# Performance work log

Measured on AMD Instinct MI355X. Metric: run time of the kernel, lower is better.

Reference implementation:

```python
import jax, jax.numpy as jnp
import numpy as np

B, IMG, P, D, NH, HS, L, V, TB, MLP, A = 32, 224, 16, 768, 12, 64, 12, 128, 32, 3072, 7
NPATCH = (IMG // P) ** 2          # 196 patches per image
SEQ = 1 + NPATCH + 1 + NPATCH + TB  # 426 = cls + obs + goal_tok + goal + lang


def _ln(x, g, b):
    m = x.mean(-1, keepdims=True)
    v = x.var(-1, keepdims=True)
    return (x - m) / jnp.sqrt(v + 1e-5) * g + b


def _patches(img):
    # einops 'b (h p1) (w p2) c -> b (h w) (p1 p2 c)'
    b = img.shape[0]
    h = IMG // P
    x = img.reshape(b, h, P, h, P, 3).transpose(0, 1, 3, 2, 4, 5)
    return x.reshape(b, h * h, P * P * 3)


def _forward(images, goal_imgs, goals_txt, patch_W, patch_b, tok_emb, pos_emb,
             cls_tok, goal_tok, Wq, Wk, Wv, Wo, bo, ln1_g, ln1_b, ln2_g, ln2_b,
             W1, b1, W2, b2, lnf_g, lnf_b, ah_W1, ah_b1, ah_W2, ah_b2):
    tok_obs = _patches(images) @ patch_W + patch_b        # [B, 196, D]
    tok_goal = _patches(goal_imgs) @ patch_W + patch_b    # [B, 196, D]
    tok_lang = tok_emb[goals_txt]                         # [B, 32, D]
    b = images.shape[0]
    x = jnp.concatenate([
        jnp.broadcast_to(cls_tok, (b, 1, D)),
        tok_obs,
        jnp.broadcast_to(goal_tok, (b, 1, D)),
        tok_goal,
        tok_lang,
    ], axis=1)                                            # [B, SEQ, D]
    x = x + pos_emb[None]
    scale = D ** -0.5  # NOTE: original Head scales by full n_embd, not head_size

    def block(x, p):
        wq, wk, wv, wo, bo_, l1g, l1b, l2g, l2b, w1, b1_, w2, b2_ = p
        xn = _ln(x, l1g, l1b)
        q = jnp.einsum('btd,hde->bhte', xn, wq)
        k = jnp.einsum('btd,hde->bhte', xn, wk)
        v = jnp.einsum('btd,hde->bhte', xn, wv)
        wei = jax.nn.softmax(jnp.einsum('bhte,bhse->bhts', q, k) * scale, axis=-1)
        att = jnp.einsum('bhts,bhse->bhte', wei, v)
        att = att.transpose(0, 2, 1, 3).reshape(x.shape[0], -1, D)  # concat heads
        x = x + att @ wo + bo_
        h = jax.nn.relu(_ln(x, l2g, l2b) @ w1 + b1_)
        x = x + h @ w2 + b2_
        return x, None

    x, _ = jax.lax.scan(block, x, (Wq, Wk, Wv, Wo, bo, ln1_g, ln1_b,
                                   ln2_g, ln2_b, W1, b1, W2, b2))
    x = _ln(x, lnf_g, lnf_b)
    cls = x[:, 0, :]
    out = jax.nn.relu(cls @ ah_W1 + ah_b1) @ ah_W2 + ah_b2  # [B, A]
    return out


def setup_inputs():
    key = jax.random.key(0)
    ks = jax.random.split(key, 20)
    nrm = lambda i, shape: 0.02 * jax.random.normal(ks[i], shape, dtype=jnp.float32)
    return {
        'images': jax.random.uniform(ks[0], (B, IMG, IMG, 3), dtype=jnp.float32),
        'goal_imgs': jax.random.uniform(ks[1], (B, IMG, IMG, 3), dtype=jnp.float32),
        'goals_txt': jax.random.randint(ks[2], (B, TB), 0, V, dtype=jnp.int32),
        'patch_W': nrm(3, (P * P * 3, D)), 'patch_b': jnp.zeros((D,), jnp.float32),
        'tok_emb': nrm(4, (V, D)),
        'pos_emb': nrm(5, (SEQ, D)),
        'cls_tok': jax.random.normal(ks[6], (1, 1, D), dtype=jnp.float32),
        'goal_tok': jax.random.normal(ks[7], (1, 1, D), dtype=jnp.float32),
        'Wq': nrm(8, (L, NH, D, HS)), 'Wk': nrm(9, (L, NH, D, HS)),
        'Wv': nrm(10, (L, NH, D, HS)),
        'Wo': nrm(11, (L, D, D)), 'bo': jnp.zeros((L, D), jnp.float32),
        'ln1_g': jnp.ones((L, D), jnp.float32), 'ln1_b': jnp.zeros((L, D), jnp.float32),
        'ln2_g': jnp.ones((L, D), jnp.float32), 'ln2_b': jnp.zeros((L, D), jnp.float32),
        'W1': nrm(12, (L, D, MLP)), 'b1': jnp.zeros((L, MLP), jnp.float32),
        'W2': nrm(13, (L, MLP, D)), 'b2': jnp.zeros((L, D), jnp.float32),
        'lnf_g': jnp.ones((D,), jnp.float32), 'lnf_b': jnp.zeros((D,), jnp.float32),
        'ah_W1': nrm(14, (D, 4 * D)), 'ah_b1': jnp.zeros((4 * D,), jnp.float32),
        'ah_W2': nrm(15, (4 * D, A)), 'ah_b2': jnp.zeros((A,), jnp.float32),
    }


def reference(images, goal_imgs, goals_txt, patch_W, patch_b, tok_emb, pos_emb,
              cls_tok, goal_tok, Wq, Wk, Wv, Wo, bo, ln1_g, ln1_b, ln2_g, ln2_b,
              W1, b1, W2, b2, lnf_g, lnf_b, ah_W1, ah_b1, ah_W2, ah_b2):
    return _forward(images, goal_imgs, goals_txt, patch_W, patch_b, tok_emb,
                    pos_emb, cls_tok, goal_tok, Wq, Wk, Wv, Wo, bo, ln1_g, ln1_b,
                    ln2_g, ln2_b, W1, b1, W2, b2, lnf_g, lnf_b, ah_W1, ah_b1,
                    ah_W2, ah_b2)
```

## Files before the change

kernel.cpp:

```cpp
#include <hip/hip_runtime.h>
#include <hip/hip_bf16.h>
#include <cstdint>

typedef __bf16 bf16x8 __attribute__((ext_vector_type(8)));
typedef __bf16 bf16x4v __attribute__((ext_vector_type(4)));
typedef float f32x4 __attribute__((ext_vector_type(4)));

static __device__ __forceinline__ f32x4 mfma16(bf16x8 a, bf16x8 b, f32x4 c) {
  return __builtin_amdgcn_mfma_f32_16x16x32_bf16(a, b, c, 0, 0, 0);
}
static __device__ __forceinline__ void gld_lds16(const void* g, void* l) {
  __builtin_amdgcn_global_load_lds(
      (__attribute__((address_space(1))) void*)(uintptr_t)g,
      (__attribute__((address_space(3))) void*)l, 16, 0, 0);
}

template <int EPI, int MODE>
__global__ __launch_bounds__(256) void gemm_bt(
    const __bf16* __restrict__ A, const __bf16* __restrict__ Bt, int K, int ldc,
    int M, int nY,
    __bf16* __restrict__ outb, float* __restrict__ outf,
    const float* __restrict__ bias, const float* __restrict__ pos) {
  __shared__ __align__(16) __bf16 lsA[128 * 32];
  __shared__ __align__(16) __bf16 lsB[128 * 32];
  const int id = blockIdx.x;
  const int xcd = id & 7;
  const int j = id >> 3;
  const int rpx = (int)gridDim.x / (8 * nY);
  int bx, by;
  if (MODE == 0) { bx = xcd * rpx + j / nY; by = j % nY; }
  else           { by = j / rpx;            bx = xcd * rpx + j % rpx; }
  const long m0 = (long)bx * 128, n0 = (long)by * 128;
  if (m0 >= M) return;

  const int tid = threadIdx.x;
  const int wave = tid >> 6, lane = tid & 63;
  const int quad = lane >> 4, l16 = lane & 15;

  const int c0 = tid, c1 = 256 + tid;
  const __bf16* gA0 = A + (m0 + (c0 >> 2)) * (long)K + (c0 & 3) * 8;
  const __bf16* gA1 = A + (m0 + (c1 >> 2)) * (long)K + (c1 & 3) * 8;
  const __bf16* gB0 = Bt + (n0 + (c0 >> 2)) * (long)K + (c0 & 3) * 8;
  const __bf16* gB1 = Bt + (n0 + (c1 >> 2)) * (long)K + (c1 & 3) * 8;
  __bf16* lA0 = lsA + wave * 512;
  __bf16* lA1 = lsA + 2048 + wave * 512;
  __bf16* lB0 = lsB + wave * 512;
  __bf16* lB1 = lsB + 2048 + wave * 512;

  const int wr = wave >> 1, wc = wave & 1;
  const __bf16* rA = lsA + (wr * 64 + l16) * 32 + quad * 8;
  const __bf16* rB = lsB + (wc * 64 + l16) * 32 + quad * 8;

  const f32x4 zz = {0.f, 0.f, 0.f, 0.f};
  f32x4 acc[4][4];
#pragma unroll
  for (int i = 0; i < 4; ++i)
#pragma unroll
    for (int jj = 0; jj < 4; ++jj) acc[i][jj] = zz;

  for (int k0 = 0; k0 < K; k0 += 32) {
    gld_lds16(gA0, lA0);
    gld_lds16(gA1, lA1);
    gld_lds16(gB0, lB0);
    gld_lds16(gB1, lB1);
    gA0 += 32; gA1 += 32; gB0 += 32; gB1 += 32;
    __syncthreads();
    bf16x8 af[4], bfr[4];
#pragma unroll
    for (int mi = 0; mi < 4; ++mi) af[mi] = *(const bf16x8*)(rA + mi * 512);
#pragma unroll
    for (int ni = 0; ni < 4; ++ni) bfr[ni] = *(const bf16x8*)(rB + ni * 512);
#pragma unroll
    for (int mi = 0; mi < 4; ++mi)
#pragma unroll
      for (int ni = 0; ni < 4; ++ni)
        acc[mi][ni] = mfma16(af[mi], bfr[ni], acc[mi][ni]);
    __syncthreads();
  }

#pragma unroll
  for (int mi = 0; mi < 4; ++mi) {
#pragma unroll
    for (int r = 0; r < 4; ++r) {
      const long row = m0 + wr * 64 + mi * 16 + quad * 4 + r;
      if (EPI == 3) {
        const int rr = (int)row;
        const int gsel = rr >= 6272 ? 1 : 0;
        const int rm = rr - gsel * 6272;
        const int bb = rm / 196, pp = rm % 196;
        const int t = gsel ? (198 + pp) : (1 + pp);
        float* xr = outf + ((long)bb * 426 + t) * 768;
        const float* pr = pos + (long)t * 768;
#pragma unroll
        for (int ni = 0; ni < 4; ++ni) {
          const long col = n0 + wc * 64 + ni * 16 + l16;
          xr[col] = acc[mi][ni][r] + bias[col] + pr[col];
        }
      } else {
#pragma unroll
        for (int ni = 0; ni < 4; ++ni) {
          const long col = n0 + wc * 64 + ni * 16 + l16;
          const float v = acc[mi][ni][r];
          if (EPI == 0) outb[row * ldc + col] = (__bf16)v;
          else if (EPI == 1) outb[row * ldc + col] = (__bf16)fmaxf(v + bias[col], 0.f);
          else outf[row * ldc + col] += v + bias[col];
        }
      }
    }
  }
}

__global__ __launch_bounds__(256) void transpose_pack(
    const float* __restrict__ in, __bf16* __restrict__ out, int K, int N,
    int nh, long out_ls, long out_hs) {
  __shared__ float tile[32][33];
  const int z = blockIdx.z;
  const long in_o = (long)z * K * N;
  const long out_o = (long)(z / nh) * out_ls + (long)(z % nh) * out_hs;
  const int n0 = blockIdx.x * 32, k0 = blockIdx.y * 32;
  const int tx = threadIdx.x, ty = threadIdx.y;
#pragma unroll
  for (int i = 0; i < 4; ++i)
    tile[ty + i * 8][tx] = in[in_o + (long)(k0 + ty + i * 8) * N + n0 + tx];
  __syncthreads();
#pragma unroll
  for (int i = 0; i < 4; ++i)
    out[out_o + (long)(n0 + ty + i * 8) * K + k0 + tx] = (__bf16)tile[tx][ty + i * 8];
}

__global__ __launch_bounds__(256) void patches_k(const float* __restrict__ img0,
                                                 const float* __restrict__ img1,
                                                 __bf16* __restrict__ out) {
  const int row = blockIdx.x;
  const int gsel = row >= 6272 ? 1 : 0;
  const int rm = row - gsel * 6272;
  const int b = rm / 196, p = rm % 196;
  const int py = p / 14, px = p % 14;
  const float* img = gsel ? img1 : img0;
#pragma unroll
  for (int i = 0; i < 3; ++i) {
    const int k = threadIdx.x + i * 256;
    const int pidx = k / 3, c = k - pidx * 3;
    const int pr = pidx >> 4, pc = pidx & 15;
    const float v = img[(((long)b * 224 + py * 16 + pr) * 224 + px * 16 + pc) * 3 + c];
    out[(long)row * 768 + k] = (__bf16)v;
  }
}

__global__ __launch_bounds__(256) void assemble_k(
    const float* __restrict__ cls_tok, const float* __restrict__ goal_tok,
    const float* __restrict__ tok_emb, const int* __restrict__ txt,
    const float* __restrict__ pos, float* __restrict__ x) {
  const int z = blockIdx.x;
  const int b = z / 34, j = z % 34;
  const int t = (j == 0) ? 0 : (j == 1) ? 197 : (392 + j);
  const float* src = (j == 0) ? cls_tok
                   : (j == 1) ? goal_tok
                              : tok_emb + (long)txt[b * 32 + (j - 2)] * 768;
  float* dst = x + ((long)b * 426 + t) * 768;
  const float* pr = pos + (long)t * 768;
#pragma unroll
  for (int i = 0; i < 3; ++i) {
    const int k = threadIdx.x + i * 256;
    dst[k] = src[k] + pr[k];
  }
}

template <int CLS>
__global__ __launch_bounds__(64) void ln_k(const float* __restrict__ x,
                                           const float* __restrict__ g,
                                           const float* __restrict__ b,
                                           __bf16* __restrict__ out) {
  const int row = blockIdx.x, lane = threadIdx.x;
  const long irow = CLS ? (long)row * 426 : (long)row;
  const float4* xr = (const float4*)(x + irow * 768);
  float4 v[3];
  float s = 0.f, q = 0.f;
#pragma unroll
  for (int i = 0; i < 3; ++i) {
    v[i] = xr[lane + i * 64];
    s += v[i].x + v[i].y + v[i].z + v[i].w;
    q += v[i].x * v[i].x + v[i].y * v[i].y + v[i].z * v[i].z + v[i].w * v[i].w;
  }
#pragma unroll
  for (int o = 32; o > 0; o >>= 1) {
    s += __shfl_xor(s, o);
    q += __shfl_xor(q, o);
  }
  const float mean = s * (1.f / 768.f);
  const float var = q * (1.f / 768.f) - mean * mean;
  const float rs = rsqrtf(var + 1e-5f);
  const float4* g4 = (const float4*)g;
  const float4* b4 = (const float4*)b;
#pragma unroll
  for (int i = 0; i < 3; ++i) {
    const float4 gg = g4[lane + i * 64], bb = b4[lane + i * 64];
    bf16x4v o4;
    o4[0] = (__bf16)((v[i].x - mean) * rs * gg.x + bb.x);
    o4[1] = (__bf16)((v[i].y - mean) * rs * gg.y + bb.y);
    o4[2] = (__bf16)((v[i].z - mean) * rs * gg.z + bb.z);
    o4[3] = (__bf16)((v[i].w - mean) * rs * gg.w + bb.w);
    *(bf16x4v*)(out + (long)row * 768 + (lane + i * 64) * 4) = o4;
  }
}

__global__ __launch_bounds__(256) void vtrans_k(const __bf16* __restrict__ qkv,
                                                __bf16* __restrict__ vt) {
  __shared__ __bf16 tile[64][66];
  const int bh = blockIdx.x;
  const int b = bh / 12, h = bh % 12;
  const int s0 = blockIdx.y * 64;
  const int t = threadIdx.x;
  const int sr = t >> 2, part = t & 3;
  const __bf16* src = qkv + ((long)(b * 426 + s0 + sr)) * 2304 + 1536 + h * 64 + part * 16;
#pragma unroll
  for (int j = 0; j < 16; ++j) tile[sr][part * 16 + j] = src[j];
  __syncthreads();
  __bf16* dst = vt + ((long)bh * 64 + sr) * 448 + s0 + part * 16;
#pragma unroll
  for (int j = 0; j < 16; ++j) {
    const int s = s0 + part * 16 + j;
    dst[j] = (s < 426) ? tile[part * 16 + j][sr] : (__bf16)0.f;
  }
}

__global__ __launch_bounds__(256) void attn_k(const __bf16* __restrict__ qkv,
                                              const __bf16* __restrict__ vt,
                                              __bf16* __restrict__ attout) {
  __shared__ __align__(16) __bf16 lds[8192 + 4096];
  const int tid = threadIdx.x;
  const int wave = tid >> 6, lane = tid & 63;
  const int quad = lane >> 4, l16 = lane & 15;
  const int bh = blockIdx.x;
  const int b = bh / 12, h = bh % 12;
  const int q0 = blockIdx.y * 64 + wave * 16;
  const long b426 = (long)b * 426;

  const int swz0 = ((quad) ^ (l16 & 7)) * 8;
  const int swz1 = ((4 + quad) ^ (l16 & 7)) * 8;
  __bf16* lsK = lds;
  __bf16* lsV = lds + 4096;
  __bf16* lsP = lds + 8192 + wave * 1024;

  const __bf16* gsrc[4];
  long gstep[4];
#pragma unroll
  for (int s = 0; s < 4; ++s) {
    const int c = s * 256 + tid;
    if (c < 512) {
      const int key = c >> 3, part = (c & 7) ^ (key & 7);
      gsrc[s] = qkv + (b426 + key) * 2304 + 768 + h * 64 + part * 8;
      gstep[s] = 64 * 2304;
    } else {
      const int cv = c - 512;
      const int e = cv >> 3, part = (cv & 7) ^ (e & 7);
      gsrc[s] = vt + ((long)bh * 64 + e) * 448 + part * 8;
      gstep[s] = 64;
    }
  }
  __bf16* ldst[4];
#pragma unroll
  for (int s = 0; s < 4; ++s) ldst[s] = lds + (s * 256 + (tid & ~63)) * 8;

  const long qrow = (b426 + q0 + l16) * 2304 + h * 64;
  const bf16x8 aq0 = *(const bf16x8*)(qkv + qrow + quad * 8);
  const bf16x8 aq1 = *(const bf16x8*)(qkv + qrow + 32 + quad * 8);

  const f32x4 zz = {0.f, 0.f, 0.f, 0.f};
  f32x4 o[4] = {zz, zz, zz, zz};
  float m_i[4] = {-3e38f, -3e38f, -3e38f, -3e38f};
  float l_i[4] = {0.f, 0.f, 0.f, 0.f};
  const float scale = 0.03608439182435161f;

  for (int kc = 0; kc < 7; ++kc) {
    const int kbase = kc * 64;
    __syncthreads();
#pragma unroll
    for (int s = 0; s < 4; ++s) {
      gld_lds16(gsrc[s], ldst[s]);
      gsrc[s] += gstep[s];
    }
    __syncthreads();

    f32x4 s4[4] = {zz, zz, zz, zz};
#pragma unroll
    for (int nt = 0; nt < 4; ++nt) {
      const __bf16* kb = lsK + (nt * 16 + l16) * 64;
      s4[nt] = mfma16(aq0, *(const bf16x8*)(kb + swz0), s4[nt]);
      s4[nt] = mfma16(aq1, *(const bf16x8*)(kb + swz1), s4[nt]);
    }

    const int lim = 426 - kbase - l16;
#pragma unroll
    for (int r = 0; r < 4; ++r) {
      float a0 = (0 < lim)  ? s4[0][r] * scale : -1e30f;
      float a1 = (16 < lim) ? s4[1][r] * scale : -1e30f;
      float a2 = (32 < lim) ? s4[2][r] * scale : -1e30f;
      float a3 = (48 < lim) ? s4[3][r] * scale : -1e30f;
      float mx = fmaxf(fmaxf(a0, a1), fmaxf(a2, a3));
#pragma unroll
      for (int w = 1; w < 16; w <<= 1) mx = fmaxf(mx, __shfl_xor(mx, w, 16));
      mx = fmaxf(mx, m_i[r]);
      const float alpha = __expf(m_i[r] - mx);
      m_i[r] = mx;
      const float p0 = __expf(a0 - mx), p1 = __expf(a1 - mx);
      const float p2 = __expf(a2 - mx), p3 = __expf(a3 - mx);
      float rs = (p0 + p1) + (p2 + p3);
#pragma unroll
      for (int w = 1; w < 16; w <<= 1) rs += __shfl_xor(rs, w, 16);
      l_i[r] = l_i[r] * alpha + rs;
      o[0][r] *= alpha; o[1][r] *= alpha; o[2][r] *= alpha; o[3][r] *= alpha;
      const int rowb = quad * 4 + r;
      __bf16* pb = lsP + rowb * 64 + (l16 & 7);
      const int l8 = l16 >> 3, rx = rowb & 7;
      pb[((0 + l8) ^ rx) * 8] = (__bf16)p0;
      pb[((2 + l8) ^ rx) * 8] = (__bf16)p1;
      pb[((4 + l8) ^ rx) * 8] = (__bf16)p2;
      pb[((6 + l8) ^ rx) * 8] = (__bf16)p3;
    }

    const bf16x8 pa0 = *(const bf16x8*)(lsP + l16 * 64 + swz0);
    const bf16x8 pa1 = *(const bf16x8*)(lsP + l16 * 64 + swz1);
#pragma unroll
    for (int et = 0; et < 4; ++et) {
      const __bf16* vb = lsV + (et * 16 + l16) * 64;
      o[et] = mfma16(pa0, *(const bf16x8*)(vb + swz0), o[et]);
      o[et] = mfma16(pa1, *(const bf16x8*)(vb + swz1), o[et]);
    }
  }

#pragma unroll
  for (int r = 0; r < 4; ++r) {
    const int q = q0 + quad * 4 + r;
    if (q < 426) {
      const float inv = 1.f / l_i[r];
      __bf16* dst = attout + (b426 + q) * 768 + h * 64 + l16;
#pragma unroll
      for (int et = 0; et < 4; ++et) dst[et * 16] = (__bf16)(o[et][r] * inv);
    }
  }
}

__global__ __launch_bounds__(256) void head1_k(const __bf16* __restrict__ cls,
                                               const float* __restrict__ W1,
                                               const float* __restrict__ b1,
                                               float* __restrict__ hh) {
  __shared__ float red[4][64];
  const int blk = blockIdx.x;
  const int r = blk / 48, nt = blk % 48;
  const int tid = threadIdx.x;
  const int kq = tid >> 6, nl = tid & 63;
  const int n = nt * 64 + nl;
  const __bf16* c = cls + (long)r * 768 + kq * 192;
  const float* w = W1 + (long)(kq * 192) * 3072 + n;
  float s = 0.f;
#pragma unroll 4
  for (int k = 0; k < 192; ++k) s += (float)c[k] * w[(long)k * 3072];
  if (kq) red[kq][nl] = s;
  __syncthreads();
  if (kq == 0) {
    s += red[1][nl] + red[2][nl] + red[3][nl];
    hh[(long)r * 3072 + n] = fmaxf(s + b1[n], 0.f);
  }
}

__global__ __launch_bounds__(64) void head2_k(const float* __restrict__ hh,
                                              const float* __restrict__ W2,
                                              const float* __restrict__ b2,
                                              float* __restrict__ out) {
  const int o = blockIdx.x;
  const int r = o / 7, n = o % 7;
  const int lane = threadIdx.x;
  const float* hr = hh + (long)r * 3072;
  float s = 0.f;
  for (int k = lane; k < 3072; k += 64) s += hr[k] * W2[(long)k * 7 + n];
#pragma unroll
  for (int off = 32; off > 0; off >>= 1) s += __shfl_xor(s, off);
  if (lane == 0) out[o] = s + b2[n];
}

extern "C" void kernel_launch(void* const* d_in, const int* in_sizes, int n_in,
                              void* d_out, int out_size, void* d_ws, size_t ws_size,
                              hipStream_t stream) {
  (void)in_sizes; (void)n_in; (void)out_size; (void)ws_size;
  const float* images   = (const float*)d_in[0];
  const float* goal_img = (const float*)d_in[1];
  const int*   txt      = (const int*)d_in[2];
  const float* patch_W  = (const float*)d_in[3];
  const float* patch_b  = (const float*)d_in[4];
  const float* tok_emb  = (const float*)d_in[5];
  const float* pos_emb  = (const float*)d_in[6];
  const float* cls_tok  = (const float*)d_in[7];
  const float* goal_tok = (const float*)d_in[8];
  const float* Wq   = (const float*)d_in[9];
  const float* Wk   = (const float*)d_in[10];
  const float* Wv   = (const float*)d_in[11];
  const float* Wo   = (const float*)d_in[12];
  const float* bo   = (const float*)d_in[13];
  const float* ln1g = (const float*)d_in[14];
  const float* ln1b = (const float*)d_in[15];
  const float* ln2g = (const float*)d_in[16];
  const float* ln2b = (const float*)d_in[17];
  const float* W1   = (const float*)d_in[18];
  const float* b1   = (const float*)d_in[19];
  const float* W2   = (const float*)d_in[20];
  const float* b2   = (const float*)d_in[21];
  const float* lnfg = (const float*)d_in[22];
  const float* lnfb = (const float*)d_in[23];
  const float* aW1  = (const float*)d_in[24];
  const float* ab1  = (const float*)d_in[25];
  const float* aW2  = (const float*)d_in[26];
  const float* ab2  = (const float*)d_in[27];

  char* base = (char*)d_ws;
  size_t off = 0;
  auto take = [&](size_t bytes) -> char* {
    char* p = base + off;
    off += (bytes + 255) & ~(size_t)255;
    return p;
  };
  float*  x     = (float*) take((size_t)13696 * 768 * 4);
  __bf16* xn    = (__bf16*)take((size_t)13696 * 768 * 2);
  __bf16* shard = (__bf16*)take((size_t)13696 * 3072 * 2);
  __bf16* attb  = (__bf16*)take((size_t)13696 * 768 * 2);
  __bf16* vt    = (__bf16*)take((size_t)384 * 64 * 448 * 2);
  float*  hh    = (float*) take((size_t)32 * 3072 * 4);
  __bf16* wqkv  = (__bf16*)take((size_t)12 * 2304 * 768 * 2);
  __bf16* wot   = (__bf16*)take((size_t)12 * 768 * 768 * 2);
  __bf16* w1t   = (__bf16*)take((size_t)12 * 768 * 3072 * 2);
  __bf16* w2t   = (__bf16*)take((size_t)12 * 768 * 3072 * 2);
  __bf16* pwt   = (__bf16*)take((size_t)768 * 768 * 2);
  __bf16* qkv   = shard;
  __bf16* hbuf  = shard;
  __bf16* patches = shard;

  const dim3 tpb(32, 8);
  transpose_pack<<<dim3(24, 24, 1), tpb, 0, stream>>>(patch_W, pwt, 768, 768, 1, 0L, 0L);
  transpose_pack<<<dim3(2, 24, 144), tpb, 0, stream>>>(Wq, wqkv, 768, 64, 12, 1769472L, 49152L);
  transpose_pack<<<dim3(2, 24, 144), tpb, 0, stream>>>(Wk, wqkv + 589824, 768, 64, 12, 1769472L, 49152L);
  transpose_pack<<<dim3(2, 24, 144), tpb, 0, stream>>>(Wv, wqkv + 1179648, 768, 64, 12, 1769472L, 49152L);
  transpose_pack<<<dim3(24, 24, 12), tpb, 0, stream>>>(Wo, wot, 768, 768, 1, 589824L, 0L);
  transpose_pack<<<dim3(96, 24, 12), tpb, 0, stream>>>(W1, w1t, 768, 3072, 1, 2359296L, 0L);
  transpose_pack<<<dim3(24, 96, 12), tpb, 0, stream>>>(W2, w2t, 3072, 768, 1, 2359296L, 0L);

  patches_k<<<12544, 256, 0, stream>>>(images, goal_img, patches);
  assemble_k<<<1088, 256, 0, stream>>>(cls_tok, goal_tok, tok_emb, txt, pos_emb, x);
  gemm_bt<3, 1><<<8 * 13 * 6, 256, 0, stream>>>(patches, pwt, 768, 768, 12544, 6,
                                                nullptr, x, patch_b, pos_emb);

  for (int l = 0; l < 12; ++l) {
    ln_k<0><<<13696, 64, 0, stream>>>(x, ln1g + l * 768, ln1b + l * 768, xn);
    gemm_bt<0, 1><<<8 * 14 * 18, 256, 0, stream>>>(xn, wqkv + (long)l * 1769472, 768, 2304,
                                                   13696, 18, qkv, nullptr, nullptr, nullptr);
    vtrans_k<<<dim3(384, 7), 256, 0, stream>>>(qkv, vt);
    attn_k<<<dim3(384, 7), 256, 0, stream>>>(qkv, vt, attb);
    gemm_bt<2, 1><<<8 * 14 * 6, 256, 0, stream>>>(attb, wot + (long)l * 589824, 768, 768,
                                                  13696, 6, nullptr, x, bo + l * 768, nullptr);
    ln_k<0><<<13696, 64, 0, stream>>>(x, ln2g + l * 768, ln2b + l * 768, xn);
    gemm_bt<1, 1><<<8 * 14 * 24, 256, 0, stream>>>(xn, w1t + (long)l * 2359296, 768, 3072,
                                                   13696, 24, hbuf, nullptr, b1 + l * 3072, nullptr);
    gemm_bt<2, 0><<<8 * 14 * 6, 256, 0, stream>>>(hbuf, w2t + (long)l * 2359296, 3072, 768,
                                                  13696, 6, nullptr, x, b2 + l * 768, nullptr);
  }
  ln_k<1><<<32, 64, 0, stream>>>(x, lnfg, lnfb, xn);
  head1_k<<<1536, 256, 0, stream>>>(xn, aW1, ab1, hh);
  head2_k<<<224, 64, 0, stream>>>(hh, aW2, ab2, (float*)d_out);
}
```

Before: 5.678 ms.

## Replace 128x128 GEMM with 256x256 tile, 4-stage LDS pipeline and swizzle

The GEMM kernel now uses 256x256 output tiles with 512 threads (8 waves, each computing 128x64), a 4-deep global_load_lds ring buffer with explicit vmcnt waits, and an XOR swizzle on LDS to reduce bank conflicts. The aim is to cut global traffic per FLOP and hide load latency, removing the two barriers per K-step of the old kernel. It adds a row bound check because 13696 and 12544 are not multiples of 256, and uses 128KB of LDS, which limits occupancy. Fewer tiles also means possible wave-quantization and tail effects on the smaller N=768 GEMMs.

```diff
diff --git a/kernel.cpp b/kernel.cpp
--- a/kernel.cpp
+++ b/kernel.cpp
@@ -16,13 +16,12 @@
 }
 
 template <int EPI, int MODE>
-__global__ __launch_bounds__(256) void gemm_bt(
+__global__ __launch_bounds__(512, 2) void gemm256(
     const __bf16* __restrict__ A, const __bf16* __restrict__ Bt, int K, int ldc,
     int M, int nY,
     __bf16* __restrict__ outb, float* __restrict__ outf,
     const float* __restrict__ bias, const float* __restrict__ pos) {
-  __shared__ __align__(16) __bf16 lsA[128 * 32];
-  __shared__ __align__(16) __bf16 lsB[128 * 32];
+  __shared__ __align__(16) __bf16 lds[4 * 16384];
   const int id = blockIdx.x;
   const int xcd = id & 7;
   const int j = id >> 3;
@@ -30,77 +29,93 @@
   int bx, by;
   if (MODE == 0) { bx = xcd * rpx + j / nY; by = j % nY; }
   else           { by = j / rpx;            bx = xcd * rpx + j % rpx; }
-  const long m0 = (long)bx * 128, n0 = (long)by * 128;
+  const long m0 = (long)bx * 256, n0 = (long)by * 256;
   if (m0 >= M) return;
 
   const int tid = threadIdx.x;
   const int wave = tid >> 6, lane = tid & 63;
   const int quad = lane >> 4, l16 = lane & 15;
-
-  const int c0 = tid, c1 = 256 + tid;
-  const __bf16* gA0 = A + (m0 + (c0 >> 2)) * (long)K + (c0 & 3) * 8;
-  const __bf16* gA1 = A + (m0 + (c1 >> 2)) * (long)K + (c1 & 3) * 8;
-  const __bf16* gB0 = Bt + (n0 + (c0 >> 2)) * (long)K + (c0 & 3) * 8;
-  const __bf16* gB1 = Bt + (n0 + (c1 >> 2)) * (long)K + (c1 & 3) * 8;
-  __bf16* lA0 = lsA + wave * 512;
-  __bf16* lA1 = lsA + 2048 + wave * 512;
-  __bf16* lB0 = lsB + wave * 512;
-  __bf16* lB1 = lsB + 2048 + wave * 512;
-
-  const int wr = wave >> 1, wc = wave & 1;
-  const __bf16* rA = lsA + (wr * 64 + l16) * 32 + quad * 8;
-  const __bf16* rB = lsB + (wc * 64 + l16) * 32 + quad * 8;
+  const int wm = wave >> 2, wn = wave & 3;
+
+  const int gc = ((lane & 3) ^ ((lane >> 3) & 3)) * 8;
+  const int srow = wave * 16 + (lane >> 2);
+  const __bf16* gA0 = A + (m0 + srow) * (long)K + gc;
+  const __bf16* gA1 = A + (m0 + 128 + srow) * (long)K + gc;
+  const __bf16* gB0 = Bt + (n0 + srow) * (long)K + gc;
+  const __bf16* gB1 = Bt + (n0 + 128 + srow) * (long)K + gc;
+  const int ldw = wave * 1024;
+
+  const int swz = (quad ^ ((l16 >> 1) & 3)) * 8;
+  const int aoff = (wm * 128 + l16) * 32 + swz;
+  const int boff = 8192 + (wn * 64 + l16) * 32 + swz;
 
   const f32x4 zz = {0.f, 0.f, 0.f, 0.f};
-  f32x4 acc[4][4];
-#pragma unroll
-  for (int i = 0; i < 4; ++i)
+  f32x4 acc[8][4];
+#pragma unroll
+  for (int i = 0; i < 8; ++i)
 #pragma unroll
     for (int jj = 0; jj < 4; ++jj) acc[i][jj] = zz;
 
-  for (int k0 = 0; k0 < K; k0 += 32) {
-    gld_lds16(gA0, lA0);
-    gld_lds16(gA1, lA1);
-    gld_lds16(gB0, lB0);
-    gld_lds16(gB1, lB1);
-    gA0 += 32; gA1 += 32; gB0 += 32; gB1 += 32;
-    __syncthreads();
-    bf16x8 af[4], bfr[4];
-#pragma unroll
-    for (int mi = 0; mi < 4; ++mi) af[mi] = *(const bf16x8*)(rA + mi * 512);
-#pragma unroll
-    for (int ni = 0; ni < 4; ++ni) bfr[ni] = *(const bf16x8*)(rB + ni * 512);
-#pragma unroll
-    for (int mi = 0; mi < 4; ++mi)
-#pragma unroll
-      for (int ni = 0; ni < 4; ++ni)
-        acc[mi][ni] = mfma16(af[mi], bfr[ni], acc[mi][ni]);
-    __syncthreads();
-  }
-
-#pragma unroll
-  for (int mi = 0; mi < 4; ++mi) {
+  const int NT = K >> 5;
+
+  auto stage = [&](int tt) {
+    char* bb = (char*)lds + (tt & 3) * 32768 + ldw;
+    const long ko = (long)tt * 32;
+    gld_lds16(gA0 + ko, bb);
+    gld_lds16(gA1 + ko, bb + 8192);
+    gld_lds16(gB0 + ko, bb + 16384);
+    gld_lds16(gB1 + ko, bb + 24576);
+  };
+
+  stage(0); stage(1); stage(2);
+  asm volatile("s_waitcnt vmcnt(8)\n\ts_barrier" ::: "memory");
+
+  for (int t = 0; t < NT; ++t) {
+    if (t + 3 < NT) stage(t + 3);
+    const __bf16* bb = lds + (t & 3) * 16384;
+    bf16x8 af[8], bf[4];
+#pragma unroll
+    for (int mf = 0; mf < 8; ++mf) af[mf] = *(const bf16x8*)(bb + aoff + mf * 512);
+#pragma unroll
+    for (int nf = 0; nf < 4; ++nf) bf[nf] = *(const bf16x8*)(bb + boff + nf * 512);
+    __builtin_amdgcn_s_setprio(1);
+#pragma unroll
+    for (int mf = 0; mf < 8; ++mf)
+#pragma unroll
+      for (int nf = 0; nf < 4; ++nf)
+        acc[mf][nf] = mfma16(af[mf], bf[nf], acc[mf][nf]);
+    __builtin_amdgcn_s_setprio(0);
+    if (t + 1 < NT) {
+      if (t + 4 <= NT)      asm volatile("s_waitcnt vmcnt(8)\n\ts_barrier" ::: "memory");
+      else if (t + 3 == NT) asm volatile("s_waitcnt vmcnt(4)\n\ts_barrier" ::: "memory");
+      else                  asm volatile("s_waitcnt vmcnt(0)\n\ts_barrier" ::: "memory");
+    }
+  }
+
+#pragma unroll
+  for (int mf = 0; mf < 8; ++mf) {
 #pragma unroll
     for (int r = 0; r < 4; ++r) {
-      const long row = m0 + wr * 64 + mi * 16 + quad * 4 + r;
+      const long row = m0 + wm * 128 + mf * 16 + quad * 4 + r;
+      if (row >= M) continue;
       if (EPI == 3) {
         const int rr = (int)row;
         const int gsel = rr >= 6272 ? 1 : 0;
         const int rm = rr - gsel * 6272;
-        const int bb = rm / 196, pp = rm % 196;
-        const int t = gsel ? (198 + pp) : (1 + pp);
-        float* xr = outf + ((long)bb * 426 + t) * 768;
-        const float* pr = pos + (long)t * 768;
-#pragma unroll
-        for (int ni = 0; ni < 4; ++ni) {
-          const long col = n0 + wc * 64 + ni * 16 + l16;
-          xr[col] = acc[mi][ni][r] + bias[col] + pr[col];
+        const int bb2 = rm / 196, pp = rm % 196;
+        const int tpos = gsel ? (198 + pp) : (1 + pp);
+        float* xr = outf + ((long)bb2 * 426 + tpos) * 768;
+        const float* pr = pos + (long)tpos * 768;
+#pragma unroll
+        for (int nf = 0; nf < 4; ++nf) {
+          const long col = n0 + wn * 64 + nf * 16 + l16;
+          xr[col] = acc[mf][nf][r] + bias[col] + pr[col];
         }
       } else {
 #pragma unroll
-        for (int ni = 0; ni < 4; ++ni) {
-          const long col = n0 + wc * 64 + ni * 16 + l16;
-          const float v = acc[mi][ni][r];
+        for (int nf = 0; nf < 4; ++nf) {
+          const long col = n0 + wn * 64 + nf * 16 + l16;
+          const float v = acc[mf][nf][r];
           if (EPI == 0) outb[row * ldc + col] = (__bf16)v;
           else if (EPI == 1) outb[row * ldc + col] = (__bf16)fmaxf(v + bias[col], 0.f);
           else outf[row * ldc + col] += v + bias[col];
@@ -445,22 +460,22 @@
 
   patches_k<<<12544, 256, 0, stream>>>(images, goal_img, patches);
   assemble_k<<<1088, 256, 0, stream>>>(cls_tok, goal_tok, tok_emb, txt, pos_emb, x);
-  gemm_bt<3, 1><<<8 * 13 * 6, 256, 0, stream>>>(patches, pwt, 768, 768, 12544, 6,
-                                                nullptr, x, patch_b, pos_emb);
+  gemm256<3, 1><<<8 * 7 * 3, 512, 0, stream>>>(patches, pwt, 768, 768, 12544, 3,
+                                               nullptr, x, patch_b, pos_emb);
 
   for (int l = 0; l < 12; ++l) {
     ln_k<0><<<13696, 64, 0, stream>>>(x, ln1g + l * 768, ln1b + l * 768, xn);
-    gemm_bt<0, 1><<<8 * 14 * 18, 256, 0, stream>>>(xn, wqkv + (long)l * 1769472, 768, 2304,
-                                                   13696, 18, qkv, nullptr, nullptr, nullptr);
+    gemm256<0, 1><<<8 * 7 * 9, 512, 0, stream>>>(xn, wqkv + (long)l * 1769472, 768, 2304,
+                                                 13696, 9, qkv, nullptr, nullptr, nullptr);
     vtrans_k<<<dim3(384, 7), 256, 0, stream>>>(qkv, vt);
     attn_k<<<dim3(384, 7), 256, 0, stream>>>(qkv, vt, attb);
-    gemm_bt<2, 1><<<8 * 14 * 6, 256, 0, stream>>>(attb, wot + (long)l * 589824, 768, 768,
-                                                  13696, 6, nullptr, x, bo + l * 768, nullptr);
+    gemm256<2, 1><<<8 * 7 * 3, 512, 0, stream>>>(attb, wot + (long)l * 589824, 768, 768,
+                                                 13696, 3, nullptr, x, bo + l * 768, nullptr);
     ln_k<0><<<13696, 64, 0, stream>>>(x, ln2g + l * 768, ln2b + l * 768, xn);
-    gemm_bt<1, 1><<<8 * 14 * 24, 256, 0, stream>>>(xn, w1t + (long)l * 2359296, 768, 3072,
-                                                   13696, 24, hbuf, nullptr, b1 + l * 3072, nullptr);
-    gemm_bt<2, 0><<<8 * 14 * 6, 256, 0, stream>>>(hbuf, w2t + (long)l * 2359296, 3072, 768,
-                                                  13696, 6, nullptr, x, b2 + l * 768, nullptr);
+    gemm256<1, 1><<<8 * 7 * 12, 512, 0, stream>>>(xn, w1t + (long)l * 2359296, 768, 3072,
+                                                  13696, 12, hbuf, nullptr, b1 + l * 3072, nullptr);
+    gemm256<2, 0><<<8 * 7 * 3, 512, 0, stream>>>(hbuf, w2t + (long)l * 2359296, 3072, 768,
+                                                 13696, 3, nullptr, x, b2 + l * 768, nullptr);
   }
   ln_k<1><<<32, 64, 0, stream>>>(x, lnfg, lnfb, xn);
   head1_k<<<1536, 256, 0, stream>>>(xn, aW1, ab1, hh);
```

After: 5.588 ms. About the same (-1.6%).
